# Performance work log

Hardware: AMD Instinct MI355X
Metric: run time of the kernel (lower is better)

Reference implementation:

```python
import jax, jax.numpy as jnp
import numpy as np

B, CIN, H, W = 4, 64, 160, 160
G, K = 8, 3
KK = K * K
PAD = K // 2
CG = CIN // G  # channels per deformable group


def setup_inputs() -> dict:
    key = jax.random.key(0)
    ks = jax.random.split(key, 6)
    x = jax.random.normal(ks[0], (B, CIN, H, W), jnp.float32)
    feat = jax.random.normal(ks[1], (B, CIN, H, W), jnp.float32)
    # conv_offset weights (zero-init in the original; small random here so offsets are nontrivial)
    w_off = jax.random.normal(ks[2], (3 * G * KK, CIN, 3, 3), jnp.float32) * 0.01
    b_off = jax.random.normal(ks[3], (3 * G * KK,), jnp.float32) * 0.01
    # deformable conv weights (torchvision DeformConv2d: groups=1, bias=True)
    w_dcn = jax.random.normal(ks[4], (CIN, CIN, K, K), jnp.float32) * (1.0 / np.sqrt(CIN * KK))
    b_dcn = jax.random.normal(ks[5], (CIN,), jnp.float32) * 0.01
    return dict(x=x, feat=feat, w_off=w_off, b_off=b_off, w_dcn=w_dcn, b_dcn=b_dcn)


def _modulated_deform_conv(x, offset, mask, w, b):
    # x: [B,C,H,W]; offset: [B,2*G*KK,H,W] (interleaved dy,dx per (g,k));
    # mask: [B,G*KK,H,W]; w: [Cout,C,K,K]; stride 1, zero padding K//2.
    Bn, C, Hh, Ww = x.shape
    off = offset.reshape(Bn, G, KK, 2, Hh, Ww)
    dy = off[:, :, :, 0]  # [B,G,KK,H,W]
    dx = off[:, :, :, 1]
    ki = jnp.arange(K)
    base_y = (jnp.repeat(ki, K) - PAD).reshape(1, 1, KK, 1, 1).astype(x.dtype)
    base_x = (jnp.tile(ki, K) - PAD).reshape(1, 1, KK, 1, 1).astype(x.dtype)
    hy = jnp.arange(Hh, dtype=x.dtype).reshape(1, 1, 1, Hh, 1)
    wx = jnp.arange(Ww, dtype=x.dtype).reshape(1, 1, 1, 1, Ww)
    py = hy + base_y + dy  # sample rows  [B,G,KK,H,W]
    px = wx + base_x + dx  # sample cols
    y0 = jnp.floor(py)
    x0 = jnp.floor(px)
    ly = py - y0
    lx = px - x0
    y0i = y0.astype(jnp.int32)
    x0i = x0.astype(jnp.int32)
    xg = x.reshape(Bn, G, CG, Hh * Ww)

    def gather(yi, xi):
        valid = ((yi >= 0) & (yi < Hh) & (xi >= 0) & (xi < Ww)).astype(x.dtype)
        idx = jnp.clip(yi, 0, Hh - 1) * Ww + jnp.clip(xi, 0, Ww - 1)
        flat = idx.reshape(Bn, G, 1, KK * Hh * Ww)
        v = jnp.take_along_axis(xg, flat, axis=3).reshape(Bn, G, CG, KK, Hh, Ww)
        return v * valid[:, :, None]  # zero padding outside

    v = ((1 - ly) * (1 - lx))[:, :, None] * gather(y0i, x0i) \
      + ((1 - ly) * lx)[:, :, None] * gather(y0i, x0i + 1) \
      + (ly * (1 - lx))[:, :, None] * gather(y0i + 1, x0i) \
      + (ly * lx)[:, :, None] * gather(y0i + 1, x0i + 1)
    v = v * mask.reshape(Bn, G, 1, KK, Hh, Ww)
    wr = w.reshape(w.shape[0], G, CG, KK)
    out = jnp.einsum('ogck,bgckhw->bohw', wr, v) + b[None, :, None, None]
    return out


def reference(x, feat, w_off, b_off, w_dcn, b_dcn):
    # conv_offset: 3x3 conv, stride 1, pad 1
    out = jax.lax.conv_general_dilated(
        feat, w_off, (1, 1), ((1, 1), (1, 1)),
        dimension_numbers=('NCHW', 'OIHW', 'NCHW')) + b_off[None, :, None, None]
    o1, o2, m = jnp.split(out, 3, axis=1)
    offset = jnp.concatenate([o1, o2], axis=1)  # [B, 2*G*KK, H, W]
    mask = jax.nn.sigmoid(m)                    # [B, G*KK, H, W]
    return _modulated_deform_conv(x, offset, mask, w_dcn, b_dcn)
```

## Files before the change

kernel.cpp:

```cpp
#include <hip/hip_runtime.h>
#include <math.h>

#define Bn   4
#define CINc 64
#define Hh   160
#define Ww   160
#define Gg   8
#define HW   (Hh * Ww)
#define COFF 216

#define OROW 220
#define VROW 200
#define OFFS_SZ (64 * OROW)
#define UNION_SZ 12800

typedef short bf16x8 __attribute__((ext_vector_type(8)));
typedef float f32x4  __attribute__((ext_vector_type(4)));

static __device__ __forceinline__ unsigned short f2bf(float f) {
    unsigned int u = __float_as_uint(f);
    u = (u + 0x7fffu + ((u >> 16) & 1u)) >> 16;
    return (unsigned short)u;
}
static __device__ __forceinline__ float bf2f(unsigned short s) {
    return __uint_as_float(((unsigned int)s) << 16);
}
static __device__ __forceinline__ float blo(unsigned int u) {
    return __uint_as_float(u << 16);
}
static __device__ __forceinline__ float bhi(unsigned int u) {
    return __uint_as_float(u & 0xffff0000u);
}

__global__ __launch_bounds__(256)
void prep_kernel(const float* __restrict__ feat, const float* __restrict__ x,
                 const float* __restrict__ w_off, const float* __restrict__ w_dcn,
                 unsigned short* __restrict__ featT, unsigned short* __restrict__ xG,
                 unsigned short* __restrict__ wofrag, unsigned short* __restrict__ wfrag) {
    const int blk = blockIdx.x;
    const int t = threadIdx.x;
    if (blk < 800) {
        const int b  = blk / 200;
        const int q  = (blk % 200) * 32 + (t >> 3);
        const int cj = t & 7;
        const float* fb = feat + (size_t)b * CINc * HW;
        float4 v[8];
        #pragma unroll
        for (int m = 0; m < 8; ++m)
            v[m] = *(const float4*)(fb + (size_t)(cj * 8 + m) * HW + q * 4);
        uint4* dst = (uint4*)featT + ((size_t)b * HW + q * 4) * 8 + cj;
        #pragma unroll
        for (int k = 0; k < 4; ++k) {
            float e[8];
            #pragma unroll
            for (int m = 0; m < 8; ++m) {
                const float4 vv = v[m];
                e[m] = (k == 0) ? vv.x : (k == 1) ? vv.y : (k == 2) ? vv.z : vv.w;
            }
            unsigned int d0, d1, d2, d3;
            asm("v_cvt_pk_bf16_f32 %0, %1, %2" : "=v"(d0) : "v"(e[0]), "v"(e[1]));
            asm("v_cvt_pk_bf16_f32 %0, %1, %2" : "=v"(d1) : "v"(e[2]), "v"(e[3]));
            asm("v_cvt_pk_bf16_f32 %0, %1, %2" : "=v"(d2) : "v"(e[4]), "v"(e[5]));
            asm("v_cvt_pk_bf16_f32 %0, %1, %2" : "=v"(d3) : "v"(e[6]), "v"(e[7]));
            uint4 r4; r4.x = d0; r4.y = d1; r4.z = d2; r4.w = d3;
            dst[(size_t)k * 8] = r4;
        }
    } else if (blk < 1600) {
        const int r  = blk - 800;
        const int bg = r / 25;
        const int q  = (r % 25) * 256 + t;
        const float* xb = x + ((size_t)(bg >> 3) * CINc + (size_t)(bg & 7) * 8) * HW;
        float4 v[8];
        #pragma unroll
        for (int cg = 0; cg < 8; ++cg)
            v[cg] = *(const float4*)(xb + (size_t)cg * HW + q * 4);
        uint4* dst = (uint4*)xG + (size_t)bg * HW + q * 4;
        #pragma unroll
        for (int k = 0; k < 4; ++k) {
            float e[8];
            #pragma unroll
            for (int cg = 0; cg < 8; ++cg) {
                const float4 vv = v[cg];
                e[cg] = (k == 0) ? vv.x : (k == 1) ? vv.y : (k == 2) ? vv.z : vv.w;
            }
            unsigned int d0, d1, d2, d3;
            asm("v_cvt_pk_bf16_f32 %0, %1, %2" : "=v"(d0) : "v"(e[0]), "v"(e[1]));
            asm("v_cvt_pk_bf16_f32 %0, %1, %2" : "=v"(d1) : "v"(e[2]), "v"(e[3]));
            asm("v_cvt_pk_bf16_f32 %0, %1, %2" : "=v"(d2) : "v"(e[4]), "v"(e[5]));
            asm("v_cvt_pk_bf16_f32 %0, %1, %2" : "=v"(d3) : "v"(e[6]), "v"(e[7]));
            uint4 r4; r4.x = d0; r4.y = d1; r4.z = d2; r4.w = d3;
            dst[k] = r4;
        }
    } else {
        for (int e = (blk - 1600) * 256 + t; e < 147456 + 36864; e += 180 * 256) {
            if (e < 147456) {
                const int j    = e & 7;
                const int lane = (e >> 3) & 63;
                const int rest = e >> 9;
                const int mt = rest & 15;
                const int q  = rest >> 4;
                const int ks = q & 1;
                const int kp = q >> 1;
                const int co = mt * 16 + (lane & 15);
                const int ci = ks * 32 + (lane >> 4) * 8 + j;
                float v = (co < COFF) ? w_off[(size_t)co * 576 + ci * 9 + kp] : 0.f;
                wofrag[e] = f2bf(v);
            } else {
                const int e2   = e - 147456;
                const int j    = e2 & 7;
                const int lane = (e2 >> 3) & 63;
                const int mt   = (e2 >> 9) & 3;
                const int ks   = e2 >> 11;
                const int m = mt * 16 + (lane & 15);
                const int k = ks * 32 + (lane >> 4) * 8 + j;
                const int g = k / 72, r = k % 72;
                const int kk = r >> 3, cg = r & 7;
                const int ci = g * 8 + cg;
                wfrag[e2] = f2bf(w_dcn[((size_t)m * CINc + ci) * 9 + kk]);
            }
        }
    }
}

#define BLEND_J(out_, w00, w01, w10, w11, c00, c01, c10, c11) {            \
    float vl_ = (c00) * blo(w00) + (c01) * blo(w01)                        \
              + (c10) * blo(w10) + (c11) * blo(w11);                       \
    float vh_ = (c00) * bhi(w00) + (c01) * bhi(w01)                        \
              + (c10) * bhi(w10) + (c11) * bhi(w11);                       \
    asm("v_cvt_pk_bf16_f32 %0, %1, %2" : "=v"(out_) : "v"(vl_), "v"(vh_)); \
}

__global__ __launch_bounds__(256, 3)
void dcnpack_fused(const unsigned short* __restrict__ featT,
                   const unsigned short* __restrict__ xG,
                   const unsigned short* __restrict__ wofrag,
                   const unsigned short* __restrict__ wfrag,
                   const float* __restrict__ b_off,
                   const float* __restrict__ b_dcn,
                   float* __restrict__ out) {
    __shared__ unsigned short smem[OFFS_SZ + UNION_SZ];
    unsigned short* offs = smem;
    unsigned short* halo = smem + OFFS_SZ;
    unsigned short* vbuf = smem + OFFS_SZ;

    const int b  = blockIdx.z;
    const int h0 = blockIdx.y * 8;
    const int w0 = blockIdx.x * 8;
    const int t  = threadIdx.x;
    const int wv   = t >> 6;
    const int lane = t & 63;
    const int n    = lane & 15;
    const int kg   = lane >> 4;

    for (int task = t; task < 800; task += 256) {
        const int pix = task >> 3, ch = task & 7;
        const int ry = pix / 10, rx = pix % 10;
        const int gh = h0 - 1 + ry, gw = w0 - 1 + rx;
        float4 v = make_float4(0.f, 0.f, 0.f, 0.f);
        if (gh >= 0 && gh < Hh && gw >= 0 && gw < Ww)
            v = *(const float4*)(featT + ((((size_t)b * Hh) + gh) * Ww + gw) * CINc + ch * 8);
        *(float4*)(halo + pix * 72 + ch * 8) = v;
    }
    __syncthreads();

    const int bbase0 = (((n >> 3) * 10) + (n & 7)) * 72 + kg * 8;

    f32x4 cacc[4][4] = {};
    bf16x8 af[3][4];
    #pragma unroll
    for (int i = 0; i < 4; ++i)
        af[0][i] = *(const bf16x8*)(wofrag + (((size_t)0 * 16 + wv + 4 * i) * 64 + lane) * 8);
    #pragma unroll
    for (int i = 0; i < 4; ++i)
        af[1][i] = *(const bf16x8*)(wofrag + (((size_t)1 * 16 + wv + 4 * i) * 64 + lane) * 8);

    #pragma unroll
    for (int s = 0; s < 18; ++s) {
        if (s + 2 < 18) {
            #pragma unroll
            for (int i = 0; i < 4; ++i)
                af[(s + 2) % 3][i] = *(const bf16x8*)(wofrag +
                    (((size_t)(s + 2) * 16 + wv + 4 * i) * 64 + lane) * 8);
        }
        const int kp = s >> 1, ks = s & 1;
        const int ky = kp / 3, kx = kp % 3;
        #pragma unroll
        for (int nt = 0; nt < 4; ++nt) {
            const bf16x8 bfr = *(const bf16x8*)(halo + bbase0 + nt * 1440 +
                                                (ky * 10 + kx) * 72 + ks * 32);
            #pragma unroll
            for (int i = 0; i < 4; ++i)
                cacc[i][nt] = __builtin_amdgcn_mfma_f32_16x16x32_bf16(af[s % 3][i], bfr, cacc[i][nt], 0, 0, 0);
        }
    }

    #pragma unroll
    for (int i = 0; i < 4; ++i) {
        const int mt = wv + 4 * i;
        #pragma unroll
        for (int r = 0; r < 4; ++r) {
            const int co = mt * 16 + kg * 4 + r;
            if (co < COFF) {
                const float bias = b_off[co];
                const int ismask = (co >= 144);
                const int gk = ismask ? (co - 144) : (co >> 1);
                const int type = ismask ? 2 : (co & 1);
                #pragma unroll
                for (int nt = 0; nt < 4; ++nt) {
                    const int p = nt * 16 + n;
                    float v = cacc[i][nt][r] + bias;
                    if (ismask) v = 1.f / (1.f + expf(-v));
                    offs[p * OROW + gk * 3 + type] = f2bf(v);
                }
            }
        }
    }
    __syncthreads();

    f32x4 dacc[4] = {};
    const int p_t = t & 63;
    const int h_s = h0 + (p_t >> 3);
    const int w_s = w0 + (p_t & 7);

    for (int c = 0; c < 3; ++c) {
        float cf[6][4];
        uint4 q[6][4];
        #pragma unroll
        for (int it = 0; it < 6; ++it) {
            const int u = c * 24 + wv + it * 4;
            const int g = u / 9;
            const int k = u % 9;

            const float dy   = bf2f(offs[p_t * OROW + u * 3 + 0]);
            const float dx   = bf2f(offs[p_t * OROW + u * 3 + 1]);
            const float mask = bf2f(offs[p_t * OROW + u * 3 + 2]);

            const float py  = (float)h_s + (float)(k / 3 - 1) + dy;
            const float pxx = (float)w_s + (float)(k % 3 - 1) + dx;
            const float y0f = floorf(py), x0f = floorf(pxx);
            const float ly = py - y0f, lx = pxx - x0f;
            const int y0 = (int)y0f, x0i = (int)x0f;
            const int y1 = y0 + 1,  x1  = x0i + 1;

            const float vy0 = (y0 >= 0 && y0 < Hh) ? 1.f : 0.f;
            const float vy1 = (y1 >= 0 && y1 < Hh) ? 1.f : 0.f;
            const float vx0 = (x0i >= 0 && x0i < Ww) ? 1.f : 0.f;
            const float vx1 = (x1 >= 0 && x1 < Ww) ? 1.f : 0.f;

            cf[it][0] = (1.f - ly) * (1.f - lx) * vy0 * vx0 * mask;
            cf[it][1] = (1.f - ly) * lx         * vy0 * vx1 * mask;
            cf[it][2] = ly         * (1.f - lx) * vy1 * vx0 * mask;
            cf[it][3] = ly         * lx         * vy1 * vx1 * mask;

            const int y0c = min(max(y0, 0), Hh - 1), y1c = min(max(y1, 0), Hh - 1);
            const int x0c = min(max(x0i, 0), Ww - 1), x1c = min(max(x1, 0), Ww - 1);

            const unsigned short* xb = xG + ((size_t)b * Gg + g) * HW * 8;
            q[it][0] = *(const uint4*)(xb + ((size_t)y0c * Ww + x0c) * 8);
            q[it][1] = *(const uint4*)(xb + ((size_t)y0c * Ww + x1c) * 8);
            q[it][2] = *(const uint4*)(xb + ((size_t)y1c * Ww + x0c) * 8);
            q[it][3] = *(const uint4*)(xb + ((size_t)y1c * Ww + x1c) * 8);
        }

        #pragma unroll
        for (int it = 0; it < 6; ++it) {
            unsigned int rr0, rr1, rr2, rr3;
            BLEND_J(rr0, q[it][0].x, q[it][1].x, q[it][2].x, q[it][3].x,
                    cf[it][0], cf[it][1], cf[it][2], cf[it][3]);
            BLEND_J(rr1, q[it][0].y, q[it][1].y, q[it][2].y, q[it][3].y,
                    cf[it][0], cf[it][1], cf[it][2], cf[it][3]);
            BLEND_J(rr2, q[it][0].z, q[it][1].z, q[it][2].z, q[it][3].z,
                    cf[it][0], cf[it][1], cf[it][2], cf[it][3]);
            BLEND_J(rr3, q[it][0].w, q[it][1].w, q[it][2].w, q[it][3].w,
                    cf[it][0], cf[it][1], cf[it][2], cf[it][3]);
            uint4 res; res.x = rr0; res.y = rr1; res.z = rr2; res.w = rr3;
            *(uint4*)(vbuf + (size_t)p_t * VROW + (wv + it * 4) * 8) = res;
        }

        bf16x8 afr[6];
        #pragma unroll
        for (int s = 0; s < 6; ++s)
            afr[s] = *(const bf16x8*)(wfrag + (((size_t)(c * 6 + s) * 4 + wv) * 64 + lane) * 8);

        __syncthreads();

        #pragma unroll
        for (int s = 0; s < 6; ++s) {
            #pragma unroll
            for (int nt = 0; nt < 4; ++nt) {
                const bf16x8 bfr = *(const bf16x8*)(vbuf + (nt * 16 + n) * VROW + s * 32 + kg * 8);
                dacc[nt] = __builtin_amdgcn_mfma_f32_16x16x32_bf16(afr[s], bfr, dacc[nt], 0, 0, 0);
            }
        }
        __syncthreads();
    }

    #pragma unroll
    for (int nt = 0; nt < 4; ++nt) {
        const int p = nt * 16 + n;
        const int h = h0 + (p >> 3);
        const int w = w0 + (p & 7);
        #pragma unroll
        for (int r = 0; r < 4; ++r) {
            const int o = wv * 16 + kg * 4 + r;
            out[(((size_t)b * CINc + o) * HW) + h * Ww + w] = dacc[nt][r] + b_dcn[o];
        }
    }
}

extern "C" void kernel_launch(void* const* d_in, const int* in_sizes, int n_in,
                              void* d_out, int out_size, void* d_ws, size_t ws_size,
                              hipStream_t stream) {
    const float* x     = (const float*)d_in[0];
    const float* feat  = (const float*)d_in[1];
    const float* w_off = (const float*)d_in[2];
    const float* b_off = (const float*)d_in[3];
    const float* w_dcn = (const float*)d_in[4];
    const float* b_dcn = (const float*)d_in[5];
    float* out = (float*)d_out;

    unsigned short* featT  = (unsigned short*)d_ws;
    unsigned short* xG     = featT + (size_t)Bn * HW * CINc;
    unsigned short* wofrag = xG + (size_t)Bn * HW * CINc;
    unsigned short* wfrag  = wofrag + (size_t)147456;

    prep_kernel<<<dim3(1780), 256, 0, stream>>>(
        feat, x, w_off, w_dcn, featT, xG, wofrag, wfrag);
    dcnpack_fused<<<dim3(Ww / 8, Hh / 8, Bn), 256, 0, stream>>>(
        featT, xG, wofrag, wfrag, b_off, b_dcn, out);
}
```

Before: 184.7 us.

## Alias offset buffer with halo in LDS and prefetch offsets to registers

Result: slower. 220.8 us (+19.6%).

```diff
diff --git a/kernel.cpp b/kernel.cpp
--- a/kernel.cpp
+++ b/kernel.cpp
@@ -9,10 +9,9 @@
 #define HW   (Hh * Ww)
 #define COFF 216
 
-#define OROW 220
 #define VROW 200
-#define OFFS_SZ (64 * OROW)
-#define UNION_SZ 12800
+#define SMEM_U32 7040
+#define MASKL_OFF_U16 9344
 
 typedef short bf16x8 __attribute__((ext_vector_type(8)));
 typedef float f32x4  __attribute__((ext_vector_type(4)));
@@ -130,7 +129,7 @@
     asm("v_cvt_pk_bf16_f32 %0, %1, %2" : "=v"(out_) : "v"(vl_), "v"(vh_)); \
 }
 
-__global__ __launch_bounds__(256, 3)
+__global__ __launch_bounds__(256, 4)
 void dcnpack_fused(const unsigned short* __restrict__ featT,
                    const unsigned short* __restrict__ xG,
                    const unsigned short* __restrict__ wofrag,
@@ -138,10 +137,11 @@
                    const float* __restrict__ b_off,
                    const float* __restrict__ b_dcn,
                    float* __restrict__ out) {
-    __shared__ unsigned short smem[OFFS_SZ + UNION_SZ];
-    unsigned short* offs = smem;
-    unsigned short* halo = smem + OFFS_SZ;
-    unsigned short* vbuf = smem + OFFS_SZ;
+    __shared__ unsigned int smem4[SMEM_U32];
+    unsigned short* halo   = (unsigned short*)smem4;
+    unsigned int*   offsYX = smem4;
+    unsigned short* maskL  = (unsigned short*)smem4 + MASKL_OFF_U16;
+    unsigned short* vbuf   = (unsigned short*)smem4;
 
     const int b  = blockIdx.z;
     const int h0 = blockIdx.y * 8;
@@ -193,47 +193,78 @@
                 cacc[i][nt] = __builtin_amdgcn_mfma_f32_16x16x32_bf16(af[s % 3][i], bfr, cacc[i][nt], 0, 0, 0);
         }
     }
+    __syncthreads();
 
     #pragma unroll
     for (int i = 0; i < 4; ++i) {
         const int mt = wv + 4 * i;
         #pragma unroll
-        for (int r = 0; r < 4; ++r) {
-            const int co = mt * 16 + kg * 4 + r;
-            if (co < COFF) {
-                const float bias = b_off[co];
-                const int ismask = (co >= 144);
-                const int gk = ismask ? (co - 144) : (co >> 1);
-                const int type = ismask ? 2 : (co & 1);
+        for (int nt = 0; nt < 4; ++nt) {
+            const int p = nt * 16 + n;
+            if (mt < 9) {
+                const int cob = mt * 16 + kg * 4;
+                const int gkA = cob >> 1;
+                const float v0 = cacc[i][nt][0] + b_off[cob + 0];
+                const float v1 = cacc[i][nt][1] + b_off[cob + 1];
+                const float v2 = cacc[i][nt][2] + b_off[cob + 2];
+                const float v3 = cacc[i][nt][3] + b_off[cob + 3];
+                unsigned int w01, w23;
+                asm("v_cvt_pk_bf16_f32 %0, %1, %2" : "=v"(w01) : "v"(v0), "v"(v1));
+                asm("v_cvt_pk_bf16_f32 %0, %1, %2" : "=v"(w23) : "v"(v2), "v"(v3));
+                offsYX[p * 73 + gkA]     = w01;
+                offsYX[p * 73 + gkA + 1] = w23;
+            } else {
                 #pragma unroll
-                for (int nt = 0; nt < 4; ++nt) {
-                    const int p = nt * 16 + n;
-                    float v = cacc[i][nt][r] + bias;
-                    if (ismask) v = 1.f / (1.f + expf(-v));
-                    offs[p * OROW + gk * 3 + type] = f2bf(v);
+                for (int r = 0; r < 4; ++r) {
+                    const int co = mt * 16 + kg * 4 + r;
+                    if (co < COFF) {
+                        float v = cacc[i][nt][r] + b_off[co];
+                        v = 1.f / (1.f + expf(-v));
+                        maskL[p * 74 + (co - 144)] = f2bf(v);
+                    }
                 }
             }
         }
     }
     __syncthreads();
 
+    const int p_t = t & 63;
+    unsigned int yx[18];
+    unsigned int mkp[9];
+    #pragma unroll
+    for (int c = 0; c < 3; ++c)
+        #pragma unroll
+        for (int it = 0; it < 6; ++it)
+            yx[c * 6 + it] = offsYX[p_t * 73 + (c * 24 + wv + it * 4)];
+    #pragma unroll
+    for (int ii = 0; ii < 9; ++ii) {
+        const int i0 = 2 * ii, i1 = 2 * ii + 1;
+        const int u0 = (i0 / 6) * 24 + wv + (i0 % 6) * 4;
+        const int u1 = (i1 / 6) * 24 + wv + (i1 % 6) * 4;
+        const unsigned int m0 = maskL[p_t * 74 + u0];
+        const unsigned int m1 = maskL[p_t * 74 + u1];
+        mkp[ii] = m0 | (m1 << 16);
+    }
+    __syncthreads();
+
     f32x4 dacc[4] = {};
-    const int p_t = t & 63;
     const int h_s = h0 + (p_t >> 3);
     const int w_s = w0 + (p_t & 7);
 
+    #pragma unroll
     for (int c = 0; c < 3; ++c) {
         float cf[6][4];
         uint4 q[6][4];
         #pragma unroll
         for (int it = 0; it < 6; ++it) {
+            const int idx = c * 6 + it;
             const int u = c * 24 + wv + it * 4;
             const int g = u / 9;
             const int k = u % 9;
 
-            const float dy   = bf2f(offs[p_t * OROW + u * 3 + 0]);
-            const float dx   = bf2f(offs[p_t * OROW + u * 3 + 1]);
-            const float mask = bf2f(offs[p_t * OROW + u * 3 + 2]);
+            const float dy   = blo(yx[idx]);
+            const float dx   = bhi(yx[idx]);
+            const float mask = (idx & 1) ? bhi(mkp[idx >> 1]) : blo(mkp[idx >> 1]);
 
             const float py  = (float)h_s + (float)(k / 3 - 1) + dy;
             const float pxx = (float)w_s + (float)(k % 3 - 1) + dx;
```

## Prefetch next chunk's bilinear gathers during MFMA and repack offset/mask LDS layout

Applied to the files above, without the earlier changes.

Measured after the change: 190.8 us. +3.3%, slower.

```diff
diff --git a/kernel.cpp b/kernel.cpp
--- a/kernel.cpp
+++ b/kernel.cpp
@@ -6,13 +6,13 @@
 #define Hh   160
 #define Ww   160
 #define Gg   8
-#define HW   (Hh * Ww)
+#define HW   (Hh * 160)
 #define COFF 216
 
-#define OROW 220
 #define VROW 200
-#define OFFS_SZ (64 * OROW)
-#define UNION_SZ 12800
+#define SMEM_U16      26880
+#define MASKL_OFF_U16 9344
+#define UNION_OFF_U16 14080
 
 typedef short bf16x8 __attribute__((ext_vector_type(8)));
 typedef float f32x4  __attribute__((ext_vector_type(4)));
@@ -130,6 +130,43 @@
     asm("v_cvt_pk_bf16_f32 %0, %1, %2" : "=v"(out_) : "v"(vl_), "v"(vh_)); \
 }
 
+#define ISSUE(cw) do {                                                        \
+    _Pragma("unroll")                                                         \
+    for (int it = 0; it < 6; ++it) {                                          \
+        const int u = (cw) * 24 + wv + it * 4;                                \
+        const int g = u / 9;                                                  \
+        const int k = u % 9;                                                  \
+        const unsigned int yx = offsYX[p_t * 73 + u];                         \
+        const float dy   = blo(yx);                                           \
+        const float dx   = bhi(yx);                                           \
+        const float mask = bf2f(maskL[p_t * 74 + u]);                         \
+        const float py  = (float)(h_s + (k / 3 - 1)) + dy;                    \
+        const float pxx = (float)(w_s + (k % 3 - 1)) + dx;                    \
+        const float y0f = floorf(py), x0f = floorf(pxx);                      \
+        const float ly = py - y0f, lx = pxx - x0f;                            \
+        const int y0 = (int)y0f, x0i = (int)x0f;                              \
+        const float vy0 = (y0 >= 0 && y0 < Hh) ? 1.f : 0.f;                   \
+        const float vy1 = (y0 >= -1 && y0 < Hh - 1) ? 1.f : 0.f;              \
+        const float vx0 = (x0i >= 0 && x0i < Ww) ? 1.f : 0.f;                 \
+        const float vx1 = (x0i >= -1 && x0i < Ww - 1) ? 1.f : 0.f;            \
+        const float m1ly = 1.f - ly, m1lx = 1.f - lx;                         \
+        cf[it][0] = m1ly * m1lx * vy0 * vx0 * mask;                           \
+        cf[it][1] = m1ly * lx   * vy0 * vx1 * mask;                           \
+        cf[it][2] = ly   * m1lx * vy1 * vx0 * mask;                           \
+        cf[it][3] = ly   * lx   * vy1 * vx1 * mask;                           \
+        const int y0c = min(max(y0, 0), Hh - 1);                              \
+        const int x0c = min(max(x0i, 0), Ww - 1);                             \
+        const int dys = (y0 >= 0 && y0 < Hh - 1) ? Ww * 8 : 0;                \
+        const int dxs = (x0i >= 0 && x0i < Ww - 1) ? 8 : 0;                   \
+        const unsigned short* xb = xG + ((size_t)b * Gg + g) * HW * 8         \
+                                 + ((size_t)y0c * Ww + x0c) * 8;              \
+        q[it][0] = *(const uint4*)(xb);                                       \
+        q[it][1] = *(const uint4*)(xb + dxs);                                 \
+        q[it][2] = *(const uint4*)(xb + dys);                                 \
+        q[it][3] = *(const uint4*)(xb + dys + dxs);                           \
+    }                                                                         \
+} while (0)
+
 __global__ __launch_bounds__(256, 3)
 void dcnpack_fused(const unsigned short* __restrict__ featT,
                    const unsigned short* __restrict__ xG,
@@ -138,10 +175,11 @@
                    const float* __restrict__ b_off,
                    const float* __restrict__ b_dcn,
                    float* __restrict__ out) {
-    __shared__ unsigned short smem[OFFS_SZ + UNION_SZ];
-    unsigned short* offs = smem;
-    unsigned short* halo = smem + OFFS_SZ;
-    unsigned short* vbuf = smem + OFFS_SZ;
+    __shared__ unsigned short smem[SMEM_U16];
+    unsigned int*   offsYX = (unsigned int*)smem;
+    unsigned short* maskL  = smem + MASKL_OFF_U16;
+    unsigned short* halo   = smem + UNION_OFF_U16;
+    unsigned short* vbuf   = smem + UNION_OFF_U16;
 
     const int b  = blockIdx.z;
     const int h0 = blockIdx.y * 8;
@@ -193,24 +231,36 @@
                 cacc[i][nt] = __builtin_amdgcn_mfma_f32_16x16x32_bf16(af[s % 3][i], bfr, cacc[i][nt], 0, 0, 0);
         }
     }
+    __syncthreads();
 
     #pragma unroll
     for (int i = 0; i < 4; ++i) {
         const int mt = wv + 4 * i;
         #pragma unroll
-        for (int r = 0; r < 4; ++r) {
-            const int co = mt * 16 + kg * 4 + r;
-            if (co < COFF) {
-                const float bias = b_off[co];
-                const int ismask = (co >= 144);
-                const int gk = ismask ? (co - 144) : (co >> 1);
-                const int type = ismask ? 2 : (co & 1);
+        for (int nt = 0; nt < 4; ++nt) {
+            const int p = nt * 16 + n;
+            if (mt < 9) {
+                const int cob = mt * 16 + kg * 4;
+                const int gkA = cob >> 1;
+                const float v0 = cacc[i][nt][0] + b_off[cob + 0];
+                const float v1 = cacc[i][nt][1] + b_off[cob + 1];
+                const float v2 = cacc[i][nt][2] + b_off[cob + 2];
+                const float v3 = cacc[i][nt][3] + b_off[cob + 3];
+                unsigned int w01, w23;
+                asm("v_cvt_pk_bf16_f32 %0, %1, %2" : "=v"(w01) : "v"(v0), "v"(v1));
+                asm("v_cvt_pk_bf16_f32 %0, %1, %2" : "=v"(w23) : "v"(v2), "v"(v3));
+                offsYX[p * 73 + gkA]     = w01;
+                offsYX[p * 73 + gkA + 1] = w23;
+            } else {
                 #pragma unroll
-                for (int nt = 0; nt < 4; ++nt) {
-                    const int p = nt * 16 + n;
-                    float v = cacc[i][nt][r] + bias;
-                    if (ismask) v = 1.f / (1.f + expf(-v));
-                    offs[p * OROW + gk * 3 + type] = f2bf(v);
+                for (int r = 0; r < 4; ++r) {
+                    const int co = mt * 16 + kg * 4 + r;
+                    if (co < COFF) {
+                        const float v = cacc[i][nt][r] + b_off[co];
+                        const float sg = __builtin_amdgcn_rcpf(
+                            1.f + __builtin_amdgcn_exp2f(v * -1.44269504f));
+                        maskL[p * 74 + (co - 144)] = f2bf(sg);
+                    }
                 }
             }
         }
@@ -222,46 +272,12 @@
     const int h_s = h0 + (p_t >> 3);
     const int w_s = w0 + (p_t & 7);
 
+    float cf[6][4];
+    uint4 q[6][4];
+    ISSUE(0);
+
+    #pragma unroll
     for (int c = 0; c < 3; ++c) {
-        float cf[6][4];
-        uint4 q[6][4];
-        #pragma unroll
-        for (int it = 0; it < 6; ++it) {
-            const int u = c * 24 + wv + it * 4;
-            const int g = u / 9;
-            const int k = u % 9;
-
-            const float dy   = bf2f(offs[p_t * OROW + u * 3 + 0]);
-            const float dx   = bf2f(offs[p_t * OROW + u * 3 + 1]);
-            const float mask = bf2f(offs[p_t * OROW + u * 3 + 2]);
-
-            const float py  = (float)h_s + (float)(k / 3 - 1) + dy;
-            const float pxx = (float)w_s + (float)(k % 3 - 1) + dx;
-            const float y0f = floorf(py), x0f = floorf(pxx);
-            const float ly = py - y0f, lx = pxx - x0f;
-            const int y0 = (int)y0f, x0i = (int)x0f;
-            const int y1 = y0 + 1,  x1  = x0i + 1;
-
-            const float vy0 = (y0 >= 0 && y0 < Hh) ? 1.f : 0.f;
-            const float vy1 = (y1 >= 0 && y1 < Hh) ? 1.f : 0.f;
-            const float vx0 = (x0i >= 0 && x0i < Ww) ? 1.f : 0.f;
-            const float vx1 = (x1 >= 0 && x1 < Ww) ? 1.f : 0.f;
-
-            cf[it][0] = (1.f - ly) * (1.f - lx) * vy0 * vx0 * mask;
-            cf[it][1] = (1.f - ly) * lx         * vy0 * vx1 * mask;
-            cf[it][2] = ly         * (1.f - lx) * vy1 * vx0 * mask;
-            cf[it][3] = ly         * lx         * vy1 * vx1 * mask;
-
-            const int y0c = min(max(y0, 0), Hh - 1), y1c = min(max(y1, 0), Hh - 1);
-            const int x0c = min(max(x0i, 0), Ww - 1), x1c = min(max(x1, 0), Ww - 1);
-
-            const unsigned short* xb = xG + ((size_t)b * Gg + g) * HW * 8;
-            q[it][0] = *(const uint4*)(xb + ((size_t)y0c * Ww + x0c) * 8);
-            q[it][1] = *(const uint4*)(xb + ((size_t)y0c * Ww + x1c) * 8);
-            q[it][2] = *(const uint4*)(xb + ((size_t)y1c * Ww + x0c) * 8);
-            q[it][3] = *(const uint4*)(xb + ((size_t)y1c * Ww + x1c) * 8);
-        }
-
         #pragma unroll
         for (int it = 0; it < 6; ++it) {
             unsigned int rr0, rr1, rr2, rr3;
@@ -284,6 +300,8 @@
 
         __syncthreads();
 
+        if (c < 2) ISSUE(c + 1);
+
         #pragma unroll
         for (int s = 0; s < 6; ++s) {
             #pragma unroll
```
